# Performance work log

Measured on AMD Instinct MI355X. Metric: run time of the kernel, lower is better.

The kernel has to match this reference:

```python
import jax, jax.numpy as jnp
import numpy as np

N, E, IN_C, EDGE_D = 100000, 1600000, 16, 4
H1, C1 = 4, 16   # conv1: heads, out channels -> 64
H2, C2 = 4, 16   # conv2: heads, out channels -> 64
G = 64           # num graphs
NUM_MIX, ACTION_DIM, GMM_HID = 3, 10, 64
NEG_SLOPE = 0.2  # PyG GATv2Conv default LeakyReLU slope


def gatv2_layer(x, src, dst, edge_attr, Wl, Wr, We, att, bias, n_nodes, heads, ch):
    # x: [N, Fin] -> out: [N, heads*ch]. Message = alpha * (Wl x)[src];
    # attention logits = att . LeakyReLU((Wl x)[src] + (Wr x)[dst] + We e).
    xl = (x @ Wl).reshape(n_nodes, heads, ch)
    xr = (x @ Wr).reshape(n_nodes, heads, ch)
    ef = (edge_attr @ We).reshape(-1, heads, ch)
    s = jax.nn.leaky_relu(xl[src] + xr[dst] + ef, NEG_SLOPE)      # [E,H,C]
    logits = jnp.einsum('ehc,hc->eh', s, att)                      # [E,H]
    m = jax.ops.segment_max(logits, dst, num_segments=n_nodes)     # [N,H]
    ex = jnp.exp(logits - m[dst])
    denom = jax.ops.segment_sum(ex, dst, num_segments=n_nodes)     # [N,H]
    alpha = ex / denom[dst]                                        # segment softmax over in-edges
    msg = alpha[..., None] * xl[src]                               # [E,H,C]
    out = jax.ops.segment_sum(msg, dst, num_segments=n_nodes)      # [N,H,C]
    return out.reshape(n_nodes, heads * ch) + bias


def global_mean_pool(x, batch, num_graphs):
    s = jax.ops.segment_sum(x, batch, num_segments=num_graphs)
    cnt = jax.ops.segment_sum(jnp.ones((x.shape[0],), x.dtype), batch, num_segments=num_graphs)
    return s / jnp.maximum(cnt, 1.0)[:, None]


def setup_inputs() -> dict:
    key = jax.random.key(0)
    ks = jax.random.split(key, 24)
    sc = 0.1
    x = jax.random.normal(ks[0], (N, IN_C), jnp.float32)
    edge_index = jax.random.randint(ks[1], (2, E), 0, N, jnp.int64)
    edge_attr = jax.random.normal(ks[2], (E, EDGE_D), jnp.float32)
    batch = jnp.sort(jax.random.randint(ks[3], (N,), 0, G, jnp.int64))
    p = {}
    p['Wl1'] = jax.random.normal(ks[4], (IN_C, H1 * C1), jnp.float32) * sc
    p['Wr1'] = jax.random.normal(ks[5], (IN_C, H1 * C1), jnp.float32) * sc
    p['We1'] = jax.random.normal(ks[6], (EDGE_D, H1 * C1), jnp.float32) * sc
    p['att1'] = jax.random.normal(ks[7], (H1, C1), jnp.float32) * sc
    p['b1'] = jnp.zeros((H1 * C1,), jnp.float32)
    p['Wl2'] = jax.random.normal(ks[8], (H1 * C1, H2 * C2), jnp.float32) * sc
    p['Wr2'] = jax.random.normal(ks[9], (H1 * C1, H2 * C2), jnp.float32) * sc
    p['We2'] = jax.random.normal(ks[10], (EDGE_D, H2 * C2), jnp.float32) * sc
    p['att2'] = jax.random.normal(ks[11], (H2, C2), jnp.float32) * sc
    p['b2'] = jnp.zeros((H2 * C2,), jnp.float32)
    p['Wg1'] = jax.random.normal(ks[12], (H2 * C2, GMM_HID), jnp.float32) * sc
    p['bg1'] = jnp.zeros((GMM_HID,), jnp.float32)
    p['Wg2'] = jax.random.normal(ks[13], (GMM_HID, NUM_MIX * 5), jnp.float32) * sc
    p['bg2'] = jnp.zeros((NUM_MIX * 5,), jnp.float32)
    p['Wp'] = jax.random.normal(ks[14], (H2 * C2, ACTION_DIM), jnp.float32) * sc
    p['bp'] = jnp.zeros((ACTION_DIM,), jnp.float32)
    p['Wc1'] = jax.random.normal(ks[15], (H2 * C2, 64), jnp.float32) * sc
    p['bc1'] = jnp.zeros((64,), jnp.float32)
    p['Wc2'] = jax.random.normal(ks[16], (64, 1), jnp.float32) * sc
    p['bc2'] = jnp.zeros((1,), jnp.float32)
    return dict(x=x, edge_index=edge_index, edge_attr=edge_attr, batch=batch, **p)


def reference(x, edge_index, edge_attr, batch,
              Wl1, Wr1, We1, att1, b1,
              Wl2, Wr2, We2, att2, b2,
              Wg1, bg1, Wg2, bg2, Wp, bp, Wc1, bc1, Wc2, bc2):
    src, dst = edge_index[0], edge_index[1]
    y = gatv2_layer(x, src, dst, edge_attr, Wl1, Wr1, We1, att1, b1, N, H1, C1)
    y = jax.nn.elu(y)
    # dropout is identity in eval mode
    y = gatv2_layer(y, src, dst, edge_attr, Wl2, Wr2, We2, att2, b2, N, H2, C2)
    g = global_mean_pool(y, batch, G)                      # [G, H2*C2]
    gmm_params = jax.nn.relu(g @ Wg1 + bg1) @ Wg2 + bg2    # [G, 15]
    num_proposals_logits = g @ Wp + bp                     # [G, 10]
    values = (jax.nn.relu(g @ Wc1 + bc1) @ Wc2 + bc2)[:, 0]  # [G]
    return gmm_params, num_proposals_logits, values
```

## Files before the change

kernel.cpp:

```cpp
#include <hip/hip_runtime.h>

#define DEVINL __device__ __forceinline__

#if __has_builtin(__builtin_amdgcn_exp2f)
DEVINL float fexp2(float x) { return __builtin_amdgcn_exp2f(x); }
#else
DEVINL float fexp2(float x) { return exp2f(x); }
#endif

DEVINL float red4(float pv) {
    pv += __int_as_float(__builtin_amdgcn_ds_swizzle(__float_as_int(pv), 0x041F));
    pv += __int_as_float(__builtin_amdgcn_ds_swizzle(__float_as_int(pv), 0x081F));
    return pv;
}

template <int K>
__global__ void k_lin_tiled(const float* __restrict__ x,
                            const float* __restrict__ Wa,
                            const float* __restrict__ Wb,
                            float* __restrict__ oa, float* __restrict__ ob,
                            int N) {
    __shared__ float sx[64 * K];
    __shared__ float sw[K * 128];
    int t = threadIdx.x;
    int base = blockIdx.x * 64;

    const int WTOT = K * 64 / 4;
    for (int i = t; i < WTOT; i += 256) {
        float4 wa = ((const float4*)Wa)[i];
        float4 wb = ((const float4*)Wb)[i];
        int k = (i * 4) >> 6, f = (i * 4) & 63;
        *(float4*)&sw[k * 128 + f] = wa;
        *(float4*)&sw[k * 128 + 64 + f] = wb;
    }
    const int XTOT = 64 * K / 4;
    for (int i = t; i < XTOT; i += 256) {
        int n = (i * 4) / K, kk = (i * 4) % K;
        float4 v = make_float4(0.f, 0.f, 0.f, 0.f);
        if (base + n < N) v = *(const float4*)&x[(size_t)(base + n) * K + kk];
        *(float4*)&sx[n * K + kk] = v;
    }
    __syncthreads();

    int fq = t & 31;
    int nq = t >> 5;
    float acc[8][4];
#pragma unroll
    for (int i = 0; i < 8; ++i)
#pragma unroll
        for (int c = 0; c < 4; ++c) acc[i][c] = 0.f;

    for (int k0 = 0; k0 < K; k0 += 4) {
        float4 xv[8];
#pragma unroll
        for (int i = 0; i < 8; ++i)
            xv[i] = *(const float4*)&sx[(nq * 8 + i) * K + k0];
#pragma unroll
        for (int kk = 0; kk < 4; ++kk) {
            float4 w = *(const float4*)&sw[(k0 + kk) * 128 + fq * 4];
#pragma unroll
            for (int i = 0; i < 8; ++i) {
                float xs = (kk == 0) ? xv[i].x : (kk == 1) ? xv[i].y
                         : (kk == 2) ? xv[i].z : xv[i].w;
                acc[i][0] = fmaf(xs, w.x, acc[i][0]);
                acc[i][1] = fmaf(xs, w.y, acc[i][1]);
                acc[i][2] = fmaf(xs, w.z, acc[i][2]);
                acc[i][3] = fmaf(xs, w.w, acc[i][3]);
            }
        }
    }

    int col = fq * 4;
    float* o = (col < 64) ? oa : ob;
    int c = col & 63;
#pragma unroll
    for (int i = 0; i < 8; ++i) {
        int n = base + nq * 8 + i;
        if (n < N)
            *(float4*)&o[(size_t)n * 64 + c] =
                make_float4(acc[i][0], acc[i][1], acc[i][2], acc[i][3]);
    }
}

__global__ void k_deg(const int* __restrict__ dst, int* __restrict__ deg, int E) {
    int e = blockIdx.x * blockDim.x + threadIdx.x;
    if (e < E) atomicAdd(&deg[dst[e]], 1);
}

__global__ void k_scan1(const int* __restrict__ deg, int* __restrict__ spart,
                        int* __restrict__ bsum, int N) {
    __shared__ int sh[256];
    int base = blockIdx.x * 1024;
    int t = threadIdx.x;
    int v[4]; int sum = 0;
#pragma unroll
    for (int i = 0; i < 4; ++i) {
        int idx = base + t * 4 + i;
        v[i] = (idx < N) ? deg[idx] : 0;
        sum += v[i];
    }
    sh[t] = sum;
    __syncthreads();
    for (int off = 1; off < 256; off <<= 1) {
        int x = (t >= off) ? sh[t - off] : 0;
        __syncthreads();
        sh[t] += x;
        __syncthreads();
    }
    int run = (t > 0) ? sh[t - 1] : 0;
#pragma unroll
    for (int i = 0; i < 4; ++i) {
        run += v[i];
        int idx = base + t * 4 + i;
        if (idx < N) spart[idx] = run;
    }
    if (t == 255) bsum[blockIdx.x] = sh[255];
}

__global__ void k_scan2(int* __restrict__ bsum, int nb) {
    __shared__ int sh[128];
    int t = threadIdx.x;
    sh[t] = (t < nb) ? bsum[t] : 0;
    __syncthreads();
    for (int off = 1; off < 128; off <<= 1) {
        int x = (t >= off) ? sh[t - off] : 0;
        __syncthreads();
        sh[t] += x;
        __syncthreads();
    }
    if (t < nb) bsum[t] = (t > 0) ? sh[t - 1] : 0;
}

__global__ void k_scan3(const int* __restrict__ spart, const int* __restrict__ bsum,
                        int* __restrict__ rowptr, int N) {
    int i = blockIdx.x * blockDim.x + threadIdx.x;
    if (i < N) rowptr[i + 1] = spart[i] + bsum[i >> 10];
    if (i == 0) rowptr[0] = 0;
}

__global__ void k_binit(const int* __restrict__ rowptr, int* __restrict__ bfill,
                        int shift, int B, int N) {
    int b = blockIdx.x * blockDim.x + threadIdx.x;
    if (b < B) {
        long long node = (long long)b << shift;
        if (node > N) node = N;
        bfill[b] = rowptr[node];
    }
}

__global__ void k_part(const int* __restrict__ src, const int* __restrict__ dst,
                       const float4* __restrict__ ea,
                       int* __restrict__ bfill, float4* __restrict__ stg,
                       int shift, int E, int chunk) {
    __shared__ int hist[512];
    __shared__ int base[512];
    int t = threadIdx.x;
    int e0 = blockIdx.x * chunk;
    int e1 = e0 + chunk; if (e1 > E) e1 = E;
    for (int i = t; i < 512; i += 256) hist[i] = 0;
    __syncthreads();
    for (int e = e0 + t; e < e1; e += 256)
        atomicAdd(&hist[(unsigned)dst[e] >> shift], 1);
    __syncthreads();
    for (int i = t; i < 512; i += 256) {
        int h = hist[i];
        base[i] = h ? atomicAdd(&bfill[i], h) : 0;
    }
    __syncthreads();
    for (int i = t; i < 512; i += 256) hist[i] = 0;
    __syncthreads();
    for (int e = e0 + t; e < e1; e += 256) {
        int d = dst[e];
        int b = (unsigned)d >> shift;
        int off = atomicAdd(&hist[b], 1);
        size_t pos = (size_t)(base[b] + off);
        stg[pos * 2] = ea[e];
        stg[pos * 2 + 1] = make_float4(__int_as_float(src[e]), __int_as_float(d), 0.f, 0.f);
    }
}

__global__ void k_scat2(const float4* __restrict__ stg,
                        const int* __restrict__ rowptr, int* __restrict__ fill,
                        float4* __restrict__ rec, int shift, int N, int E) {
    int b = blockIdx.x;
    long long n0 = (long long)b << shift; if (n0 > N) n0 = N;
    long long n1 = (long long)(b + 1) << shift; if (n1 > N) n1 = N;
    int s0 = rowptr[n0], s1 = rowptr[n1];
    for (int i = s0 + (int)threadIdx.x; i < s1; i += 256) {
        float4 a = stg[(size_t)i * 2];
        float4 meta = stg[(size_t)i * 2 + 1];
        int d = __float_as_int(meta.y);
        int pos = rowptr[d] + atomicAdd(&fill[d], 1);
        rec[(size_t)pos * 2] = a;
        rec[(size_t)pos * 2 + 1] = make_float4(meta.x, 0.f, 0.f, 0.f);
    }
}

__global__ void k_scatter(const int* __restrict__ src, const int* __restrict__ dst,
                          const float4* __restrict__ ea,
                          const int* __restrict__ rowptr, int* __restrict__ fill,
                          float4* __restrict__ rec, int E) {
    int e = blockIdx.x * blockDim.x + threadIdx.x;
    if (e >= E) return;
    int d = dst[e];
    float4 a = ea[e];
    int s = src[e];
    int pos = rowptr[d] + atomicAdd(&fill[d], 1);
    rec[(size_t)pos * 2] = a;
    rec[(size_t)pos * 2 + 1] = make_float4(__int_as_float(s), 0.f, 0.f, 0.f);
}

__global__ void k_gat_agg(const int* __restrict__ rowptr,
                          const float4* __restrict__ rec,
                          const float* __restrict__ xl,
                          const float* __restrict__ xr,
                          const float* __restrict__ We,
                          const float* __restrict__ att,
                          const float* __restrict__ bias,
                          float* __restrict__ out,
                          int N, int elu) {
    int l = threadIdx.x & 63;
    int n = blockIdx.x * 4 + (threadIdx.x >> 6);
    if (n >= N) return;
    int q = l & 15;
    int g = l >> 4;
    int f4 = q * 4;
    const float LOG2E = 1.44269504088896f;

    float4 w0 = *(const float4*)&We[f4];
    float4 w1 = *(const float4*)&We[64 + f4];
    float4 w2 = *(const float4*)&We[128 + f4];
    float4 w3 = *(const float4*)&We[192 + f4];
    float4 at = *(const float4*)&att[f4];
    at.x *= LOG2E; at.y *= LOG2E; at.z *= LOG2E; at.w *= LOG2E;
    float4 xr4 = *(const float4*)&xr[(size_t)n * 64 + f4];

    int beg = rowptr[n], end = rowptr[n + 1];
    const float4* xl4 = (const float4*)xl;

    float m = -1e30f, den = 0.f;
    float4 acc = make_float4(0.f, 0.f, 0.f, 0.f);

    for (int jb = beg; jb < end; jb += 4) {
        int j = jb + g;
        bool valid = (j < end);
        int jj = valid ? j : end - 1;
        float4 a = rec[(size_t)jj * 2];
        int s = *(const int*)(rec + (size_t)jj * 2 + 1);
        float4 xv = xl4[(unsigned)s * 16u + (unsigned)q];
        float vx = fmaf(a.x, w0.x, fmaf(a.y, w1.x, fmaf(a.z, w2.x, fmaf(a.w, w3.x, xr4.x)))) + xv.x;
        float vy = fmaf(a.x, w0.y, fmaf(a.y, w1.y, fmaf(a.z, w2.y, fmaf(a.w, w3.y, xr4.y)))) + xv.y;
        float vz = fmaf(a.x, w0.z, fmaf(a.y, w1.z, fmaf(a.z, w2.z, fmaf(a.w, w3.z, xr4.z)))) + xv.z;
        float vw = fmaf(a.x, w0.w, fmaf(a.y, w1.w, fmaf(a.z, w2.w, fmaf(a.w, w3.w, xr4.w)))) + xv.w;
        vx = fmaxf(vx, 0.2f * vx);
        vy = fmaxf(vy, 0.2f * vy);
        vz = fmaxf(vz, 0.2f * vz);
        vw = fmaxf(vw, 0.2f * vw);
        float pv = fmaf(vx, at.x, fmaf(vy, at.y, fmaf(vz, at.z, vw * at.w)));
        pv = red4(pv);
        pv = valid ? pv : -3.0e38f;
        float mn = fmaxf(m, pv);
        float sc = fexp2(m - mn);
        float e  = fexp2(pv - mn);
        den = fmaf(den, sc, e);
        acc.x = fmaf(e, xv.x, acc.x * sc);
        acc.y = fmaf(e, xv.y, acc.y * sc);
        acc.z = fmaf(e, xv.z, acc.z * sc);
        acc.w = fmaf(e, xv.w, acc.w * sc);
        m = mn;
    }

#pragma unroll
    for (int mask = 16; mask <= 32; mask <<= 1) {
        float m2 = __shfl_xor(m, mask);
        float d2 = __shfl_xor(den, mask);
        float ax = __shfl_xor(acc.x, mask);
        float ay = __shfl_xor(acc.y, mask);
        float az = __shfl_xor(acc.z, mask);
        float aw = __shfl_xor(acc.w, mask);
        float mn = fmaxf(m, m2);
        float s1 = fexp2(m - mn);
        float s2 = fexp2(m2 - mn);
        den = den * s1 + d2 * s2;
        acc.x = acc.x * s1 + ax * s2;
        acc.y = acc.y * s1 + ay * s2;
        acc.z = acc.z * s1 + az * s2;
        acc.w = acc.w * s1 + aw * s2;
        m = mn;
    }

    float inv = (den > 0.f) ? 1.f / den : 0.f;
    float4 b4 = *(const float4*)&bias[f4];
    float4 val;
    val.x = fmaf(acc.x, inv, b4.x);
    val.y = fmaf(acc.y, inv, b4.y);
    val.z = fmaf(acc.z, inv, b4.z);
    val.w = fmaf(acc.w, inv, b4.w);
    if (elu) {
        val.x = (val.x > 0.f) ? val.x : expm1f(val.x);
        val.y = (val.y > 0.f) ? val.y : expm1f(val.y);
        val.z = (val.z > 0.f) ? val.z : expm1f(val.z);
        val.w = (val.w > 0.f) ? val.w : expm1f(val.w);
    }
    if (l < 16) ((float4*)out)[(size_t)n * 16 + q] = val;
}

__global__ void k_pool(const float* __restrict__ y2,
                       const int* __restrict__ batch,
                       float* __restrict__ pool, float* __restrict__ cnt, int N) {
    const int CH = 256;
    int f = threadIdx.x & 63;
    int lane = threadIdx.x >> 6;
    int base = blockIdx.x * CH;
    int curg = -1;
    float acc = 0.f;
    float c = 0.f;
    for (int n = base + lane; n < base + CH && n < N; n += 4) {
        int g = batch[n];
        if (g != curg) {
            if (curg >= 0) {
                atomicAdd(pool + (size_t)curg * 64 + f, acc);
                if (f == 0) atomicAdd(cnt + curg, c);
            }
            curg = g; acc = 0.f; c = 0.f;
        }
        acc += y2[(size_t)n * 64 + f];
        c += 1.f;
    }
    if (curg >= 0) {
        atomicAdd(pool + (size_t)curg * 64 + f, acc);
        if (f == 0) atomicAdd(cnt + curg, c);
    }
}

__global__ void k_head(const float* __restrict__ pool, const float* __restrict__ cnt,
                       const float* __restrict__ Wg1, const float* __restrict__ bg1,
                       const float* __restrict__ Wg2, const float* __restrict__ bg2,
                       const float* __restrict__ Wp, const float* __restrict__ bp,
                       const float* __restrict__ Wc1, const float* __restrict__ bc1,
                       const float* __restrict__ Wc2, const float* __restrict__ bc2,
                       float* __restrict__ out) {
    int g = blockIdx.x, f = threadIdx.x;
    __shared__ float sg[64];
    __shared__ float sh[64];
    float inv = 1.f / fmaxf(cnt[g], 1.f);
    sg[f] = pool[(size_t)g * 64 + f] * inv;
    __syncthreads();
    float acc = bg1[f];
    for (int k = 0; k < 64; ++k) acc += sg[k] * Wg1[k * 64 + f];
    sh[f] = fmaxf(acc, 0.f);
    __syncthreads();
    if (f < 15) {
        float o = bg2[f];
        for (int k = 0; k < 64; ++k) o += sh[k] * Wg2[k * 15 + f];
        out[(size_t)g * 15 + f] = o;
    }
    if (f < 10) {
        float o = bp[f];
        for (int k = 0; k < 64; ++k) o += sg[k] * Wp[k * 10 + f];
        out[960 + (size_t)g * 10 + f] = o;
    }
    __syncthreads();
    float acc2 = bc1[f];
    for (int k = 0; k < 64; ++k) acc2 += sg[k] * Wc1[k * 64 + f];
    sh[f] = fmaxf(acc2, 0.f);
    __syncthreads();
    if (f == 0) {
        float v = bc2[0];
        for (int k = 0; k < 64; ++k) v += sh[k] * Wc2[k];
        out[1600 + g] = v;
    }
}

extern "C" void kernel_launch(void* const* d_in, const int* in_sizes, int n_in,
                              void* d_out, int out_size, void* d_ws, size_t ws_size,
                              hipStream_t stream) {
    const float* x     = (const float*)d_in[0];
    const int*   ei    = (const int*)d_in[1];
    const float* ea    = (const float*)d_in[2];
    const int*   batch = (const int*)d_in[3];
    const float* Wl1 = (const float*)d_in[4];
    const float* Wr1 = (const float*)d_in[5];
    const float* We1 = (const float*)d_in[6];
    const float* att1 = (const float*)d_in[7];
    const float* b1  = (const float*)d_in[8];
    const float* Wl2 = (const float*)d_in[9];
    const float* Wr2 = (const float*)d_in[10];
    const float* We2 = (const float*)d_in[11];
    const float* att2 = (const float*)d_in[12];
    const float* b2  = (const float*)d_in[13];
    const float* Wg1 = (const float*)d_in[14];
    const float* bg1 = (const float*)d_in[15];
    const float* Wg2 = (const float*)d_in[16];
    const float* bg2 = (const float*)d_in[17];
    const float* Wp  = (const float*)d_in[18];
    const float* bp  = (const float*)d_in[19];
    const float* Wc1 = (const float*)d_in[20];
    const float* bc1 = (const float*)d_in[21];
    const float* Wc2 = (const float*)d_in[22];
    const float* bc2 = (const float*)d_in[23];

    const int N = in_sizes[0] / 16;
    const int E = in_sizes[2] / 4;
    const int* src = ei;
    const int* dst = ei + E;

    int shift = 8;
    while (((N + (1 << shift) - 1) >> shift) > 512) ++shift;
    int B = (N + (1 << shift) - 1) >> shift;

    size_t NF = (size_t)N * 64;
    size_t tail = ((size_t)(N + 1) + N + N + 128 + 513 + 4096 + 64) * 4;
    size_t need = 3 * NF * 4 + (size_t)E * 32 + tail;
    bool radix = (ws_size >= need) && (2 * NF * 4 >= (size_t)E * 32);

    char* w = (char*)d_ws;
    float* A = (float*)w; w += NF * 4;
    float* B_ = (float*)w; w += NF * 4;
    float* C = (float*)w; w += NF * 4;
    float4* rec = (float4*)w; w += (size_t)E * 32;
    int* rowptr = (int*)w; w += (size_t)(N + 1) * 4;
    int* deg    = (int*)w; w += (size_t)N * 4;
    int* spart  = (int*)w; w += (size_t)N * 4;
    int* bsum   = (int*)w; w += 128 * 4;
    int* bfill  = (int*)w; w += 513 * 4;
    float* PL   = (float*)w; w += 4096 * 4;
    float* CT   = (float*)w;
    float4* stg = (float4*)A;

    dim3 blk(256);
    int gE  = (E + 255) / 256;
    int gN  = (N + 255) / 256;
    int nb1 = (N + 1023) / 1024;
    int gAgg = (N + 3) / 4;
    int gLin = (N + 63) / 64;

    hipMemsetAsync(deg, 0, (size_t)N * sizeof(int), stream);
    k_deg<<<gE, blk, 0, stream>>>(dst, deg, E);
    k_scan1<<<nb1, blk, 0, stream>>>(deg, spart, bsum, N);
    k_scan2<<<1, 128, 0, stream>>>(bsum, nb1);
    k_scan3<<<gN, blk, 0, stream>>>(spart, bsum, rowptr, N);
    hipMemsetAsync(deg, 0, (size_t)N * sizeof(int), stream);
    if (radix) {
        k_binit<<<(B + 255) / 256, blk, 0, stream>>>(rowptr, bfill, shift, B, N);
        int gridA = 512;
        int chunk = (E + gridA - 1) / gridA;
        k_part<<<gridA, blk, 0, stream>>>(src, dst, (const float4*)ea, bfill,
                                          stg, shift, E, chunk);
        k_scat2<<<B, blk, 0, stream>>>(stg, rowptr, deg, rec, shift, N, E);
    } else {
        k_scatter<<<gE, blk, 0, stream>>>(src, dst, (const float4*)ea,
                                          rowptr, deg, rec, E);
    }

    k_lin_tiled<16><<<gLin, blk, 0, stream>>>(x, Wl1, Wr1, A, B_, N);
    k_gat_agg<<<gAgg, blk, 0, stream>>>(rowptr, rec, A, B_, We1, att1, b1, C, N, 1);

    k_lin_tiled<64><<<gLin, blk, 0, stream>>>(C, Wl2, Wr2, B_, A, N);
    k_gat_agg<<<gAgg, blk, 0, stream>>>(rowptr, rec, B_, A, We2, att2, b2, C, N, 0);

    hipMemsetAsync(PL, 0, (4096 + 64) * sizeof(float), stream);
    k_pool<<<(N + 255) / 256, blk, 0, stream>>>(C, batch, PL, CT, N);
    k_head<<<64, 64, 0, stream>>>(PL, CT, Wg1, bg1, Wg2, bg2, Wp, bp,
                                  Wc1, bc1, Wc2, bc2, (float*)d_out);
}
```

Baseline: 485.3 us.

## Shrink CSR edge records to (src, edge id) and gather edge_attr in aggregation

The radix partition staging record is packed into one 64-bit word (edge id, src, low dst bits) instead of two float4s. The final CSR holds only an int2 (src, edge id) instead of a 32-byte record with copied edge attributes. This cuts write and read traffic in the partition and scatter passes and shrinks the CSR read in both aggregation passes. In exchange, each aggregation edge now does a random gather of edge_attr by edge id, which is less coalesced than the old sequential record read. The new bit packing also limits the radix path to E < 2^24 and shift <= 12.

New measurement: 460.7 us. 1.05x faster.

```diff
diff --git a/kernel.cpp b/kernel.cpp
--- a/kernel.cpp
+++ b/kernel.cpp
@@ -149,8 +149,7 @@
 }
 
 __global__ void k_part(const int* __restrict__ src, const int* __restrict__ dst,
-                       const float4* __restrict__ ea,
-                       int* __restrict__ bfill, float4* __restrict__ stg,
+                       int* __restrict__ bfill, unsigned long long* __restrict__ stg,
                        int shift, int E, int chunk) {
     __shared__ int hist[512];
     __shared__ int base[512];
@@ -169,49 +168,50 @@
     __syncthreads();
     for (int i = t; i < 512; i += 256) hist[i] = 0;
     __syncthreads();
+    unsigned mask = (1u << shift) - 1u;
     for (int e = e0 + t; e < e1; e += 256) {
         int d = dst[e];
         int b = (unsigned)d >> shift;
         int off = atomicAdd(&hist[b], 1);
-        size_t pos = (size_t)(base[b] + off);
-        stg[pos * 2] = ea[e];
-        stg[pos * 2 + 1] = make_float4(__int_as_float(src[e]), __int_as_float(d), 0.f, 0.f);
-    }
-}
-
-__global__ void k_scat2(const float4* __restrict__ stg,
+        unsigned long long p = ((unsigned long long)(unsigned)e << 40)
+                             | ((unsigned long long)(unsigned)src[e] << 12)
+                             | (unsigned long long)((unsigned)d & mask);
+        stg[(size_t)(base[b] + off)] = p;
+    }
+}
+
+__global__ void k_scat2(const unsigned long long* __restrict__ stg,
                         const int* __restrict__ rowptr, int* __restrict__ fill,
-                        float4* __restrict__ rec, int shift, int N, int E) {
+                        int2* __restrict__ csr, int shift, int N) {
     int b = blockIdx.x;
     long long n0 = (long long)b << shift; if (n0 > N) n0 = N;
     long long n1 = (long long)(b + 1) << shift; if (n1 > N) n1 = N;
     int s0 = rowptr[n0], s1 = rowptr[n1];
+    unsigned mask = (1u << shift) - 1u;
     for (int i = s0 + (int)threadIdx.x; i < s1; i += 256) {
-        float4 a = stg[(size_t)i * 2];
-        float4 meta = stg[(size_t)i * 2 + 1];
-        int d = __float_as_int(meta.y);
+        unsigned long long p = stg[i];
+        int dlow = (int)(p & mask);
+        int s = (int)((p >> 12) & 0xFFFFFFFu);
+        int eid = (int)(p >> 40);
+        int d = (b << shift) | dlow;
         int pos = rowptr[d] + atomicAdd(&fill[d], 1);
-        rec[(size_t)pos * 2] = a;
-        rec[(size_t)pos * 2 + 1] = make_float4(meta.x, 0.f, 0.f, 0.f);
+        csr[pos] = make_int2(s, eid);
     }
 }
 
 __global__ void k_scatter(const int* __restrict__ src, const int* __restrict__ dst,
-                          const float4* __restrict__ ea,
                           const int* __restrict__ rowptr, int* __restrict__ fill,
-                          float4* __restrict__ rec, int E) {
+                          int2* __restrict__ csr, int E) {
     int e = blockIdx.x * blockDim.x + threadIdx.x;
     if (e >= E) return;
     int d = dst[e];
-    float4 a = ea[e];
-    int s = src[e];
     int pos = rowptr[d] + atomicAdd(&fill[d], 1);
-    rec[(size_t)pos * 2] = a;
-    rec[(size_t)pos * 2 + 1] = make_float4(__int_as_float(s), 0.f, 0.f, 0.f);
+    csr[pos] = make_int2(src[e], e);
 }
 
 __global__ void k_gat_agg(const int* __restrict__ rowptr,
-                          const float4* __restrict__ rec,
+                          const int2* __restrict__ csr,
+                          const float4* __restrict__ ea,
                           const float* __restrict__ xl,
                           const float* __restrict__ xr,
                           const float* __restrict__ We,
@@ -245,9 +245,9 @@
         int j = jb + g;
         bool valid = (j < end);
         int jj = valid ? j : end - 1;
-        float4 a = rec[(size_t)jj * 2];
-        int s = *(const int*)(rec + (size_t)jj * 2 + 1);
-        float4 xv = xl4[(unsigned)s * 16u + (unsigned)q];
+        int2 se = csr[jj];
+        float4 a = ea[(unsigned)se.y];
+        float4 xv = xl4[(unsigned)se.x * 16u + (unsigned)q];
         float vx = fmaf(a.x, w0.x, fmaf(a.y, w1.x, fmaf(a.z, w2.x, fmaf(a.w, w3.x, xr4.x)))) + xv.x;
         float vy = fmaf(a.x, w0.y, fmaf(a.y, w1.y, fmaf(a.z, w2.y, fmaf(a.w, w3.y, xr4.y)))) + xv.y;
         float vz = fmaf(a.x, w0.z, fmaf(a.y, w1.z, fmaf(a.z, w2.z, fmaf(a.w, w3.z, xr4.z)))) + xv.z;
@@ -408,17 +408,14 @@
     int shift = 8;
     while (((N + (1 << shift) - 1) >> shift) > 512) ++shift;
     int B = (N + (1 << shift) - 1) >> shift;
+    bool radix = (shift <= 12) && (N <= (1 << 28)) && (E < (1 << 24));
 
     size_t NF = (size_t)N * 64;
-    size_t tail = ((size_t)(N + 1) + N + N + 128 + 513 + 4096 + 64) * 4;
-    size_t need = 3 * NF * 4 + (size_t)E * 32 + tail;
-    bool radix = (ws_size >= need) && (2 * NF * 4 >= (size_t)E * 32);
-
     char* w = (char*)d_ws;
-    float* A = (float*)w; w += NF * 4;
+    float* A  = (float*)w; w += NF * 4;
     float* B_ = (float*)w; w += NF * 4;
-    float* C = (float*)w; w += NF * 4;
-    float4* rec = (float4*)w; w += (size_t)E * 32;
+    float* C  = (float*)w; w += NF * 4;
+    int2* csr = (int2*)w;  w += (size_t)E * 8;
     int* rowptr = (int*)w; w += (size_t)(N + 1) * 4;
     int* deg    = (int*)w; w += (size_t)N * 4;
     int* spart  = (int*)w; w += (size_t)N * 4;
@@ -426,7 +423,8 @@
     int* bfill  = (int*)w; w += 513 * 4;
     float* PL   = (float*)w; w += 4096 * 4;
     float* CT   = (float*)w;
-    float4* stg = (float4*)A;
+    unsigned long long* stg = (unsigned long long*)A;
+    radix = radix && ((size_t)E * 8 <= NF * 4);
 
     dim3 blk(256);
     int gE  = (E + 255) / 256;
@@ -445,19 +443,19 @@
         k_binit<<<(B + 255) / 256, blk, 0, stream>>>(rowptr, bfill, shift, B, N);
         int gridA = 512;
         int chunk = (E + gridA - 1) / gridA;
-        k_part<<<gridA, blk, 0, stream>>>(src, dst, (const float4*)ea, bfill,
-                                          stg, shift, E, chunk);
-        k_scat2<<<B, blk, 0, stream>>>(stg, rowptr, deg, rec, shift, N, E);
+        k_part<<<gridA, blk, 0, stream>>>(src, dst, bfill, stg, shift, E, chunk);
+        k_scat2<<<B, blk, 0, stream>>>(stg, rowptr, deg, csr, shift, N);
     } else {
-        k_scatter<<<gE, blk, 0, stream>>>(src, dst, (const float4*)ea,
-                                          rowptr, deg, rec, E);
+        k_scatter<<<gE, blk, 0, stream>>>(src, dst, rowptr, deg, csr, E);
     }
 
     k_lin_tiled<16><<<gLin, blk, 0, stream>>>(x, Wl1, Wr1, A, B_, N);
-    k_gat_agg<<<gAgg, blk, 0, stream>>>(rowptr, rec, A, B_, We1, att1, b1, C, N, 1);
+    k_gat_agg<<<gAgg, blk, 0, stream>>>(rowptr, csr, (const float4*)ea, A, B_,
+                                        We1, att1, b1, C, N, 1);
 
     k_lin_tiled<64><<<gLin, blk, 0, stream>>>(C, Wl2, Wr2, B_, A, N);
-    k_gat_agg<<<gAgg, blk, 0, stream>>>(rowptr, rec, B_, A, We2, att2, b2, C, N, 0);
+    k_gat_agg<<<gAgg, blk, 0, stream>>>(rowptr, csr, (const float4*)ea, B_, A,
+                                        We2, att2, b2, C, N, 0);
 
     hipMemsetAsync(PL, 0, (4096 + 64) * sizeof(float), stream);
     k_pool<<<(N + 255) / 256, blk, 0, stream>>>(C, batch, PL, CT, N);
```
